# Kernel tuning notes

Measured on AMD Instinct MI355X. Metric: run time of the kernel, lower is better.

## Reference

```python
import jax, jax.numpy as jnp
import numpy as np

N_NODES = 50000


def gcn_conv(x, W, b, src, dst, ew, n):
    """PyG-style GCNConv: D^-1/2 (A+I) D^-1/2 X W + b with self-loops of weight 1."""
    h = x @ W                                   # [N, out]
    loop = jnp.arange(n, dtype=src.dtype)
    s = jnp.concatenate([src, loop])            # [E+N]
    d = jnp.concatenate([dst, loop])
    w = jnp.concatenate([ew, jnp.ones((n,), dtype=x.dtype)])
    deg = jax.ops.segment_sum(w, d, num_segments=n)
    dinv = jnp.where(deg > 0, jax.lax.rsqrt(deg), 0.0)
    norm = dinv[s] * w * dinv[d]                # [E+N]
    out = jax.ops.segment_sum(h[s] * norm[:, None], d, num_segments=n)
    return out + b


def setup_inputs() -> dict:
    key = jax.random.key(0)
    ks = jax.random.split(key, 12)
    in_feats, hidden = 128, 128
    half = hidden // 2
    E = 800000
    x = jax.random.normal(ks[0], (N_NODES, in_feats), dtype=jnp.float32)
    edge_index = jax.random.randint(ks[1], (2, E), 0, N_NODES, dtype=jnp.int64)
    edge_weight = jax.random.uniform(ks[2], (E,), dtype=jnp.float32)
    def lin(k, fan_in, shape):
        bound = 1.0 / np.sqrt(fan_in)
        return jax.random.uniform(k, shape, minval=-bound, maxval=bound, dtype=jnp.float32)
    return {
        "x": x,
        "edge_index": edge_index,
        "edge_weight": edge_weight,
        "W1": lin(ks[3], in_feats, (in_feats, hidden)),
        "b1": jnp.zeros((hidden,), jnp.float32),
        "W2": lin(ks[4], hidden, (hidden, hidden)),
        "b2": jnp.zeros((hidden,), jnp.float32),
        "Ws": lin(ks[5], in_feats, (in_feats, hidden)),
        "bs": lin(ks[6], in_feats, (hidden,)),
        "Wl": lin(ks[7], in_feats, (in_feats, half)),
        "bl": jnp.zeros((half,), jnp.float32),
        "Wl2": lin(ks[8], half, (half, 1)),
        "bl2": lin(ks[9], half, (1,)),
    }


def reference(x, edge_index, edge_weight, W1, b1, W2, b2, Ws, bs, Wl, bl, Wl2, bl2):
    n = x.shape[0]
    src, dst = edge_index[0], edge_index[1]
    # conv1 + ReLU over neighbors
    h_neighbors = jax.nn.relu(gcn_conv(x, W1, b1, src, dst, edge_weight, n))
    # leader score: GCNConv -> ReLU -> Linear(.,1) -> sigmoid, per node
    ls_h = jax.nn.relu(gcn_conv(x, Wl, bl, src, dst, edge_weight, n))
    leader_score = jax.nn.sigmoid(ls_h @ Wl2 + bl2)        # [N, 1]
    # gated fusion of self projection vs neighbor aggregation
    h_self_proj = x @ Ws + bs
    h_new = (1.0 - leader_score) * h_neighbors + leader_score * h_self_proj
    h_final = jax.nn.relu(gcn_conv(h_new, W2, b2, src, dst, edge_weight, n))
    return (h_final, leader_score)
```

## Files before the change

kernel.cpp:

```cpp
#include <hip/hip_runtime.h>
#include <math.h>

#define THREADS 256
#define ELLS 96
#define GEMM_YSTRIDE 104
#define NPHA 256
#define BSHIFT 7
#define NBMAX 392
#define BCAP 4096
#define PERMAX 3136
#define PMAX 5872
#define LMAX 736

typedef unsigned int uint32;
typedef unsigned long long ull64;
typedef __attribute__((ext_vector_type(8))) short bf16x8;
typedef __attribute__((ext_vector_type(4))) float f32x4;
typedef __attribute__((ext_vector_type(2))) float f32x2;

__device__ __forceinline__ unsigned short f2bf_rne(float x) {
  uint32 u = __float_as_uint(x);
  u += 0x7fffu + ((u >> 16) & 1u);
  return (unsigned short)(u >> 16);
}

__device__ __forceinline__ f32x2 dw2f2(uint32 d) {
  f32x2 r;
  r.x = __uint_as_float(d << 16);
  r.y = __uint_as_float(d & 0xffff0000u);
  return r;
}


__global__ __launch_bounds__(256) void prep_fused(uint32* __restrict__ gcnt, int n,
                                                  const float* __restrict__ W1, const float* __restrict__ Wl,
                                                  const float* __restrict__ Ws, const float* __restrict__ W2,
                                                  unsigned short* __restrict__ whi, unsigned short* __restrict__ wlo,
                                                  const float* __restrict__ x, unsigned short* __restrict__ xraw,
                                                  int nW) {
  int b = blockIdx.x;
  int t = threadIdx.x;
  if (b == 0) {
    for (int k = t; k < NBMAX; k += 256) gcnt[k] = 0u;
// ... 9 lines not shown
    else if (slot < 192) { W = Wl; ncol = slot - 128; ncols = 64;  }
    else if (slot < 320) { W = Ws; ncol = slot - 192; ncols = 128; }
    else                 { W = W2; ncol = slot - 320; ncols = 128; }
    float v = W[(size_t)k * ncols + ncol];
    unsigned short hi = f2bf_rne(v);
    float hif = __uint_as_float((uint32)hi << 16);
    unsigned short lo = f2bf_rne(v - hif);
    whi[idx] = hi;
    wlo[idx] = lo;
  } else {
    int i = (b - 1 - nW) * 256 + t;
    if (i >= n * 16) return;
    const float* px = x + (size_t)i * 8;
    float4 a = *(const float4*)px;
    float4 c = *(const float4*)(px + 4);
    ushort4 r0, r1;
    r0.x = f2bf_rne(a.x); r0.y = f2bf_rne(a.y); r0.z = f2bf_rne(a.z); r0.w = f2bf_rne(a.w);
    r1.x = f2bf_rne(c.x); r1.y = f2bf_rne(c.y); r1.z = f2bf_rne(c.z); r1.w = f2bf_rne(c.w);
    *(ushort4*)(xraw + (size_t)i * 8) = r0;
    *(ushort4*)(xraw + (size_t)i * 8 + 4) = r1;
  }
}


struct Chunk {
  const unsigned short* A;
  const unsigned short* whi;
  const unsigned short* wlo;
  const float* bias;
  void* out;
  int ostride;
  int obf16;
};
struct GemmArgs { Chunk c[5]; };

__device__ __forceinline__ void gemm_body(const Chunk& d, int M, int nTiles, int tile0, int tstride) {
  const unsigned short* A = d.A;
  int w = threadIdx.x >> 6, lane = threadIdx.x & 63;
  int n16 = lane & 15, quad = lane >> 4;

  bf16x8 Bh[4][4], Bl[4][4];
  {
    const unsigned short* wh = d.whi + (size_t)n16 * 128 + quad * 8;
    const unsigned short* wl = d.wlo + (size_t)n16 * 128 + quad * 8;
#pragma unroll
    for (int ct = 0; ct < 4; ct++)
#pragma unroll
      for (int ks = 0; ks < 4; ks++) {
        Bh[ct][ks] = *(const bf16x8*)(wh + ct * 16 * 128 + ks * 32);
        Bl[ct][ks] = *(const bf16x8*)(wl + ct * 16 * 128 + ks * 32);
      }
  }
  float bv[4];
#pragma unroll
  for (int ct = 0; ct < 4; ct++) bv[ct] = d.bias ? d.bias[ct * 16 + n16] : 0.f;

  int tile = tile0;
  bf16x8 av0[4], av1[4];
  if (tile < nTiles) {
    int bm = tile * 128;
    int r0 = bm + w * 32 + n16, r1 = r0 + 16;
    int r0c = r0 < M ? r0 : M - 1;
    int r1c = r1 < M ? r1 : M - 1;
    const unsigned short* a0 = A + (size_t)r0c * 128 + quad * 8;
    const unsigned short* a1 = A + (size_t)r1c * 128 + quad * 8;
#pragma unroll
    for (int ks = 0; ks < 4; ks++) {
// ... 30 lines not shown
#pragma unroll
      for (int ct = 0; ct < 4; ct++) {
        acc[0][ct] = __builtin_amdgcn_mfma_f32_16x16x32_bf16(av0[ks], Bh[ct][ks], acc[0][ct], 0, 0, 0);
        acc[0][ct] = __builtin_amdgcn_mfma_f32_16x16x32_bf16(av0[ks], Bl[ct][ks], acc[0][ct], 0, 0, 0);
        acc[1][ct] = __builtin_amdgcn_mfma_f32_16x16x32_bf16(av1[ks], Bh[ct][ks], acc[1][ct], 0, 0, 0);
        acc[1][ct] = __builtin_amdgcn_mfma_f32_16x16x32_bf16(av1[ks], Bl[ct][ks], acc[1][ct], 0, 0, 0);
      }

    int bm = tile * 128;
#pragma unroll
    for (int ct = 0; ct < 4; ct++) {
      int col = ct * 16 + n16;
#pragma unroll
      for (int rt = 0; rt < 2; rt++) {
#pragma unroll
        for (int reg = 0; reg < 4; reg++) {
          int row = bm + w * 32 + rt * 16 + quad * 4 + reg;
          if (row < M) {
            float v = acc[rt][ct][reg] + bv[ct];
            if (d.obf16)
              ((unsigned short*)d.out)[(size_t)row * d.ostride + col] = f2bf_rne(v);
            else
              ((float*)d.out)[(size_t)row * d.ostride + col] = v;
          }
        }
      }
    }

#pragma unroll
    for (int ks = 0; ks < 4; ks++) { av0[ks] = nv0[ks]; av1[ks] = nv1[ks]; }
  }
}

__global__ __launch_bounds__(256, 2) void gemm_v3(GemmArgs args, int M, int nTiles) {
  gemm_body(args.c[blockIdx.x], M, nTiles, blockIdx.y, gridDim.y);
}


__global__ __launch_bounds__(256, 2) void fused_sg(GemmArgs args, int M, int nTiles, int nGemm,
                                                   const int* __restrict__ ei, const float* __restrict__ ew,
                                                   uint32* __restrict__ gcnt, uint2* __restrict__ staging, int E) {
  __shared__ uint32 cntS[NBMAX], offS[NBMAX], gbS[NBMAX], curS[NBMAX];
  __shared__ unsigned short lineBk[LMAX];
  __shared__ uint2 sortedS[PMAX];
  __shared__ uint32 Ptot;

  int b = blockIdx.x;
  int gemmIdx = -1, phIdx = -1;
  int twice = NPHA * 2;
  if (b < twice) {
    if (b & 1) gemmIdx = b >> 1; else phIdx = b >> 1;
  } else {
    gemmIdx = NPHA + (b - twice);
  }

  if (phIdx >= 0) {
    int t = threadIdx.x;
    int per = (E + NPHA - 1) / NPHA;
    int start = phIdx * per;
    int end = start + per; if (end > E) end = E;
    for (int k = t; k < NBMAX; k += 256) cntS[k] = 0u;
    __syncthreads();
    for (int i = start + t; i < end; i += 256)
      atomicAdd(&cntS[(uint32)ei[E + i] >> BSHIFT], 1u);
    __syncthreads();
    if (t < 64) {
      uint32 carry = 0;
      for (int base = 0; base < NBMAX; base += 64) {
        int k = base + t;
        uint32 v = (k < NBMAX) ? ((cntS[k] + 7u) & ~7u) : 0u;
        uint32 s = v;
#pragma unroll
        for (int dd = 1; dd < 64; dd <<= 1) {
          uint32 o = __shfl_up(s, dd);
          if (t >= dd) s += o;
        }
        if (k < NBMAX) offS[k] = carry + s - v;
        carry += __shfl(s, 63);
      }
      if (t == 0) Ptot = carry;
    }
    __syncthreads();
    uint32 P = Ptot;
    for (int k = t; k < NBMAX; k += 256) {
      uint32 pc = (cntS[k] + 7u) & ~7u;
      gbS[k] = pc ? atomicAdd(&gcnt[k], pc) : 0u;
      curS[k] = 0u;
      uint32 l1 = (offS[k] + pc) >> 3;
      for (uint32 l = offS[k] >> 3; l < l1; l++) lineBk[l] = (unsigned short)k;
    }
    for (uint32 j = t; j < P; j += 256) sortedS[j] = make_uint2(0xFFFFFFFFu, 0u);
    __syncthreads();
    for (int i = start + t; i < end; i += 256) {
      int d = ei[E + i];
      int s = ei[i];
      float w = ew[i];
      int bk = d >> BSHIFT;
      uint32 pos = offS[bk] + atomicAdd(&curS[bk], 1u);
      sortedS[pos] = make_uint2(((uint32)(d & 127) << 24) | (uint32)s, __float_as_uint(w));
    }
    __syncthreads();
    for (uint32 j = t; j < P; j += 256) {
      int k = lineBk[j >> 3];
      uint32 idx = gbS[k] + (j - offS[k]);
      if (idx < BCAP)
        staging[(size_t)k * BCAP + idx] = sortedS[j];
    }
    return;
  }

  int chunkId = gemmIdx % 5;
  int ytile = gemmIdx / 5;
  gemm_body(args.c[chunkId], M, nTiles, ytile, GEMM_YSTRIDE);
}


__global__ __launch_bounds__(256) void phaseB_kernel(const uint2* __restrict__ staging,
                                                     const uint32* __restrict__ gcnt,
                                                     int2* __restrict__ ell,
                                                     float* __restrict__ dinv, int* __restrict__ cnt32, int n) {
  __shared__ uint32 cntL[128], sumL[128];
  int b = blockIdx.x;
  int t = threadIdx.x;
  if (t < 128) { cntL[t] = 0u; sumL[t] = 0u; }
  __syncthreads();
  uint32 cnt = gcnt[b]; if (cnt > BCAP) cnt = BCAP;
  const uint2* sb = staging + (size_t)b * BCAP;
  int dbase = b << BSHIFT;
  for (uint32 i = t; i < cnt; i += 256) {
    uint2 en = sb[i];
    if ((en.x >> 24) == 0xFFu) continue;
    int dl = (int)(en.x >> 24);
    int s = (int)(en.x & 0xffffffu);
    float w = __uint_as_float(en.y);
    uint32 fx = (uint32)(w * 8388608.0f + 0.5f);
    atomicAdd(&sumL[dl], fx);
    uint32 slot = atomicAdd(&cntL[dl], 1u);
    if (slot < ELLS)
      ell[(size_t)(dbase + dl) * ELLS + slot] = make_int2(s, __float_as_int(w));
  }
  __syncthreads();
  if (t < 128) {
    int d = dbase + t;
    if (d < n) {
      const float S = 1.1920928955078125e-7f;
      dinv[d] = rsqrtf(1.0f + (float)sumL[t] * S);
      uint32 c = cntL[t];
      cnt32[d] = (int)(c < ELLS ? c : ELLS);
    }
  }
}


__global__ __launch_bounds__(256) void conv1_fused(const unsigned short* __restrict__ h1,
                                                   const unsigned short* __restrict__ hl,
                                                   const int* __restrict__ cnt,
                                                   const int2* __restrict__ csr,
                                                   const float* __restrict__ dinv,
                                                   const float* __restrict__ b1, const float* __restrict__ bl,
                                                   const float* __restrict__ Wl2, const float* __restrict__ bl2,
                                                   const unsigned short* __restrict__ hself,
                                                   unsigned short* __restrict__ hnew_out,
                                                   float* __restrict__ leader_out, int nnodes) {
  int wave = threadIdx.x >> 6;
  int lane = threadIdx.x & 63;
  int node = blockIdx.x * 4 + wave;
  if (node >= nnodes) return;
  int g = lane >> 4, q = lane & 15;
  bool ql = q < 8;
  int hq = q & 7;
  int rs = node * ELLS;
  int n = cnt[node];
  float di = dinv[node];
  f32x2 dv2 = {di, di};

  f32x2 acc1[4] = {};
  f32x2 accl[4] = {};
  if (g == 0) {
    uint4 v = *(const uint4*)(h1 + (size_t)node * 128 + 8 * q);
    acc1[0] = dv2 * dw2f2(v.x); acc1[1] = dv2 * dw2f2(v.y);
    acc1[2] = dv2 * dw2f2(v.z); acc1[3] = dv2 * dw2f2(v.w);
    if (ql) {
      uint4 vl = *(const uint4*)(hl + (size_t)node * 64 + 8 * q);
      accl[0] = dv2 * dw2f2(vl.x); accl[1] = dv2 * dw2f2(vl.y);
      accl[2] = dv2 * dw2f2(vl.z); accl[3] = dv2 * dw2f2(vl.w);
    }
  }

  int e = g;
  for (; e + 4 < n; e += 8) {
    int2 en0 = csr[rs + e];
    int2 en1 = csr[rs + e + 4];
    float wz0 = __int_as_float(en0.y) * dinv[en0.x];
    float wz1 = __int_as_float(en1.y) * dinv[en1.x];
    f32x2 w0 = {wz0, wz0};
    f32x2 w1 = {wz1, wz1};
    uint4 a0 = *(const uint4*)(h1 + (size_t)en0.x * 128 + 8 * q);
    uint4 a1 = *(const uint4*)(h1 + (size_t)en1.x * 128 + 8 * q);
    int srcl = ql ? en0.x : en1.x;
    float wzl = ql ? wz0 : wz1;
    uint4 c0 = *(const uint4*)(hl + (size_t)srcl * 64 + 8 * hq);
    f32x2 wl2 = {wzl, wzl};
    accl[0] += wl2 * dw2f2(c0.x);
    accl[1] += wl2 * dw2f2(c0.y);
    accl[2] += wl2 * dw2f2(c0.z);
    accl[3] += wl2 * dw2f2(c0.w);
    acc1[0] += w0 * dw2f2(a0.x) + w1 * dw2f2(a1.x);
    acc1[1] += w0 * dw2f2(a0.y) + w1 * dw2f2(a1.y);
    acc1[2] += w0 * dw2f2(a0.z) + w1 * dw2f2(a1.z);
    acc1[3] += w0 * dw2f2(a0.w) + w1 * dw2f2(a1.w);
  }
  if (e < n) {
    int2 en = csr[rs + e];
    float wz0 = __int_as_float(en.y) * dinv[en.x];
    f32x2 w0 = {wz0, wz0};
    uint4 a0 = *(const uint4*)(h1 + (size_t)en.x * 128 + 8 * q);
    float wzl = ql ? wz0 : 0.f;
    uint4 c0 = *(const uint4*)(hl + (size_t)en.x * 64 + 8 * hq);
    f32x2 wl2 = {wzl, wzl};
    accl[0] += wl2 * dw2f2(c0.x);
    accl[1] += wl2 * dw2f2(c0.y);
    accl[2] += wl2 * dw2f2(c0.z);
    accl[3] += wl2 * dw2f2(c0.w);
    acc1[0] += w0 * dw2f2(a0.x);
    acc1[1] += w0 * dw2f2(a0.y);
    acc1[2] += w0 * dw2f2(a0.z);
    acc1[3] += w0 * dw2f2(a0.w);
  }

#pragma unroll
  for (int k = 0; k < 4; k++) {
    acc1[k].x += __shfl_xor(acc1[k].x, 16);
    acc1[k].y += __shfl_xor(acc1[k].y, 16);
    acc1[k].x += __shfl_xor(acc1[k].x, 32);
    acc1[k].y += __shfl_xor(acc1[k].y, 32);
    accl[k].x += __shfl_xor(accl[k].x, 16);
    accl[k].y += __shfl_xor(accl[k].y, 16);
    accl[k].x += __shfl_xor(accl[k].x, 32);
    accl[k].y += __shfl_xor(accl[k].y, 32);
    accl[k].x += __shfl_xor(accl[k].x, 8);
    accl[k].y += __shfl_xor(accl[k].y, 8);
  }

  float part = 0.f;
  if (ql) {
    float b[8], w2[8];
    *(float4*)&b[0] = *(const float4*)(bl + 8 * q);
    *(float4*)&b[4] = *(const float4*)(bl + 8 * q + 4);
    *(float4*)&w2[0] = *(const float4*)(Wl2 + 8 * q);
    *(float4*)&w2[4] = *(const float4*)(Wl2 + 8 * q + 4);
#pragma unroll
    for (int k = 0; k < 4; k++) {
      part += fmaxf(di * accl[k].x + b[2 * k], 0.f) * w2[2 * k];
      part += fmaxf(di * accl[k].y + b[2 * k + 1], 0.f) * w2[2 * k + 1];
    }
  }
  part += __shfl_xor(part, 1);
  part += __shfl_xor(part, 2);
  part += __shfl_xor(part, 4);
  float z = __shfl(part, 0) + bl2[0];
  float l = 1.f / (1.f + expf(-z));
  if (lane == 0) leader_out[node] = l;

  if (g == 0) {
    float b[8], r[8], hs[8];
    *(float4*)&b[0] = *(const float4*)(b1 + 8 * q);
    *(float4*)&b[4] = *(const float4*)(b1 + 8 * q + 4);
    uint4 hsv = *(const uint4*)(hself + (size_t)node * 128 + 8 * q);
    f32x2 h0 = dw2f2(hsv.x), h1v = dw2f2(hsv.y), h2v = dw2f2(hsv.z), h3v = dw2f2(hsv.w);
    hs[0] = h0.x; hs[1] = h0.y; hs[2] = h1v.x; hs[3] = h1v.y;
    hs[4] = h2v.x; hs[5] = h2v.y; hs[6] = h3v.x; hs[7] = h3v.y;
    float a[8];
    a[0] = acc1[0].x; a[1] = acc1[0].y; a[2] = acc1[1].x; a[3] = acc1[1].y;
    a[4] = acc1[2].x; a[5] = acc1[2].y; a[6] = acc1[3].x; a[7] = acc1[3].y;
#pragma unroll
    for (int j = 0; j < 8; j++) {
      r[j] = fmaxf(di * a[j] + b[j], 0.f);
      r[j] = (1.f - l) * r[j] + l * hs[j];
      r[j] *= di;
    }
    ushort4 p0, p1;
    p0.x = f2bf_rne(r[0]); p0.y = f2bf_rne(r[1]); p0.z = f2bf_rne(r[2]); p0.w = f2bf_rne(r[3]);
    p1.x = f2bf_rne(r[4]); p1.y = f2bf_rne(r[5]); p1.z = f2bf_rne(r[6]); p1.w = f2bf_rne(r[7]);
    *(ushort4*)(hnew_out + (size_t)node * 128 + 8 * q) = p0;
    *(ushort4*)(hnew_out + (size_t)node * 128 + 8 * q + 4) = p1;
  }
}


__global__ __launch_bounds__(256) void agg_conv2_kernel(const unsigned short* __restrict__ h,
                                                        const int* __restrict__ cnt,
                                                        const int2* __restrict__ csr,
                                                        const float* __restrict__ dinv, const float* __restrict__ bias,
                                                        float* __restrict__ out, int nnodes) {
  int wave = threadIdx.x >> 6;
  int lane = threadIdx.x & 63;
  int node = blockIdx.x * 4 + wave;
  if (node >= nnodes) return;
  int g = lane >> 4;
  int q = lane & 15;
  int rs = node * ELLS;
  int n = cnt[node];
  float di = dinv[node];

  f32x2 acc[4] = {};
  if (g == 0) {
    uint4 v = *(const uint4*)(h + (size_t)node * 128 + 8 * q);
    acc[0] = dw2f2(v.x); acc[1] = dw2f2(v.y);
    acc[2] = dw2f2(v.z); acc[3] = dw2f2(v.w);
  }
  int e = g;
  for (; e + 4 < n; e += 8) {
    int2 en0 = csr[rs + e];
    int2 en1 = csr[rs + e + 4];
    f32x2 w0 = {__int_as_float(en0.y), __int_as_float(en0.y)};
    f32x2 w1 = {__int_as_float(en1.y), __int_as_float(en1.y)};
    uint4 v0 = *(const uint4*)(h + (size_t)en0.x * 128 + 8 * q);
    uint4 v1 = *(const uint4*)(h + (size_t)en1.x * 128 + 8 * q);
// ... 36 lines not shown
extern "C" void kernel_launch(void* const* d_in, const int* in_sizes, int n_in,
                              void* d_out, int out_size, void* d_ws, size_t ws_size,
                              hipStream_t stream) {
  const float* x   = (const float*)d_in[0];
  const int*   ei  = (const int*)d_in[1];
  const float* ew  = (const float*)d_in[2];
  const float* W1  = (const float*)d_in[3];
  const float* b1  = (const float*)d_in[4];
  const float* W2  = (const float*)d_in[5];
  const float* b2  = (const float*)d_in[6];
  const float* Wsp = (const float*)d_in[7];
  const float* bs  = (const float*)d_in[8];
  const float* Wl  = (const float*)d_in[9];
  const float* bl  = (const float*)d_in[10];
  const float* Wl2 = (const float*)d_in[11];
  const float* bl2 = (const float*)d_in[12];

  const int N = in_sizes[0] / 128;
  const int E = in_sizes[1] / 2;
  const int NB = (N + 127) >> BSHIFT;

  char* ws = (char*)d_ws;
  size_t off = 0;
  auto alloc = [&](size_t bytes) -> void* {
    void* p = ws + off;
    off = (off + bytes + 255) & ~(size_t)255;
    return p;
  };
  uint32* gcnt     = (uint32*)alloc((size_t)NBMAX * 4);
  uint2* staging   = (uint2*)alloc((size_t)NBMAX * BCAP * 8);
  float* dinv      = (float*)alloc((size_t)N * 4);
  int*   cnt32     = (int*)alloc((size_t)N * 4);
  int2*  ell       = (int2*)alloc((size_t)N * ELLS * 8);
  unsigned short* xraw   = (unsigned short*)alloc((size_t)N * 128 * 2);
  unsigned short* h1bf   = (unsigned short*)alloc((size_t)N * 128 * 2);
  unsigned short* hlbf   = (unsigned short*)alloc((size_t)N * 64 * 2);
  unsigned short* hnewbf = (unsigned short*)alloc((size_t)N * 128 * 2);
  unsigned short* hspbf  = (unsigned short*)alloc((size_t)N * 128 * 2);
  unsigned short* whi = (unsigned short*)alloc((size_t)448 * 128 * 2);
  unsigned short* wlo = (unsigned short*)alloc((size_t)448 * 128 * 2);

  float* h_final = (float*)d_out;
  float* leader  = (float*)d_out + (size_t)N * 128;

  int gWave = (N + 3) / 4;
  int nTiles = (N + 127) / 128;
  int nCast = (N * 16 + 255) / 256;
  int nW = (448 * 128 + 255) / 256;

  prep_fused<<<1 + nW + nCast, 256, 0, stream>>>(gcnt, N, W1, Wl, Wsp, W2, whi, wlo, x, xraw, nW);

  {
    GemmArgs ga;
    ga.c[0] = {xraw, whi + 0 * 128,   wlo + 0 * 128,   nullptr, h1bf,       128, 1};
    ga.c[1] = {xraw, whi + 64 * 128,  wlo + 64 * 128,  nullptr, h1bf + 64,  128, 1};
    ga.c[2] = {xraw, whi + 128 * 128, wlo + 128 * 128, nullptr, hlbf,       64,  1};
    ga.c[3] = {xraw, whi + 192 * 128, wlo + 192 * 128, bs,      hspbf,      128, 1};
    ga.c[4] = {xraw, whi + 256 * 128, wlo + 256 * 128, bs + 64, hspbf + 64, 128, 1};
    int nGemm = 5 * GEMM_YSTRIDE;
    int totalBlocks = NPHA * 2 + (nGemm - NPHA);
    fused_sg<<<totalBlocks, 256, 0, stream>>>(ga, N, nTiles, nGemm, ei, ew, gcnt, staging, E);
  }

  phaseB_kernel<<<NB, 256, 0, stream>>>(staging, gcnt, ell, dinv, cnt32, N);

  conv1_fused<<<gWave, 256, 0, stream>>>(h1bf, hlbf, cnt32, ell, dinv,
                                         b1, bl, Wl2, bl2, hspbf, hnewbf, leader, N);

  {
    GemmArgs ga;
    ga.c[0] = {hnewbf, whi + 320 * 128, wlo + 320 * 128, nullptr, h1bf,      128, 1};
    ga.c[1] = {hnewbf, whi + 384 * 128, wlo + 384 * 128, nullptr, h1bf + 64, 128, 1};
    ga.c[2] = ga.c[0]; ga.c[3] = ga.c[0]; ga.c[4] = ga.c[0];
    gemm_v3<<<dim3(2, 256), 256, 0, stream>>>(ga, N, nTiles);
  }
  agg_conv2_kernel<<<gWave, 256, 0, stream>>>(h1bf, cnt32, ell,
                                              dinv, b2, h_final, N);
}
```

Measured before the change: 254.0 us.

## Fuse conv2 GEMM into conv1 aggregation epilogue via LDS tile and MFMA

The conv1 aggregation kernel now processes 16 nodes per block and stages the gated h_new rows in shared memory. It then multiplies them by W2 with bf16 MFMA (hi/lo split) directly, writing h2. This drops the separate GEMM launch and the round trip of h_new through global memory. In exchange, each block reloads the W2 fragments from global memory and adds a block barrier, and each wave now serially handles four nodes, so less latency is hidden per wave.

```diff
diff --git a/kernel.cpp b/kernel.cpp
--- a/kernel.cpp
+++ b/kernel.cpp
@@ -8,7 +8,6 @@
 #define BSHIFT 7
 #define NBMAX 392
 #define BCAP 4096
-#define PERMAX 3136
 #define PMAX 5872
 #define LMAX 736
 
@@ -181,10 +180,6 @@
   }
 }
 
-__global__ __launch_bounds__(256, 2) void gemm_v3(GemmArgs args, int M, int nTiles) {
-  gemm_body(args.c[blockIdx.x], M, nTiles, blockIdx.y, gridDim.y);
-}
-
 
 __global__ __launch_bounds__(256, 2) void fused_sg(GemmArgs args, int M, int nTiles, int nGemm,
                                                    const int* __restrict__ ei, const float* __restrict__ ew,
@@ -301,138 +296,180 @@
 }
 
 
-__global__ __launch_bounds__(256) void conv1_fused(const unsigned short* __restrict__ h1,
-                                                   const unsigned short* __restrict__ hl,
-                                                   const int* __restrict__ cnt,
-                                                   const int2* __restrict__ csr,
-                                                   const float* __restrict__ dinv,
-                                                   const float* __restrict__ b1, const float* __restrict__ bl,
-                                                   const float* __restrict__ Wl2, const float* __restrict__ bl2,
-                                                   const unsigned short* __restrict__ hself,
-                                                   unsigned short* __restrict__ hnew_out,
-                                                   float* __restrict__ leader_out, int nnodes) {
+__global__ __launch_bounds__(256) void conv1_g2(const unsigned short* __restrict__ h1,
+                                                const unsigned short* __restrict__ hl,
+                                                const int* __restrict__ cnt,
+                                                const int2* __restrict__ csr,
+                                                const float* __restrict__ dinv,
+                                                const float* __restrict__ b1, const float* __restrict__ bl,
+                                                const float* __restrict__ Wl2, const float* __restrict__ bl2,
+                                                const unsigned short* __restrict__ hself,
+                                                const unsigned short* __restrict__ whi,
+                                                const unsigned short* __restrict__ wlo,
+                                                unsigned short* __restrict__ h2_out,
+                                                float* __restrict__ leader_out, int nnodes) {
+  __shared__ unsigned short hn[16][136];
+  int blk = blockIdx.x;
   int wave = threadIdx.x >> 6;
   int lane = threadIdx.x & 63;
-  int node = blockIdx.x * 4 + wave;
-  if (node >= nnodes) return;
   int g = lane >> 4, q = lane & 15;
   bool ql = q < 8;
   int hq = q & 7;
-  int rs = node * ELLS;
-  int n = cnt[node];
-  float di = dinv[node];
-  f32x2 dv2 = {di, di};
-
-  f32x2 acc1[4] = {};
-  f32x2 accl[4] = {};
-  if (g == 0) {
-    uint4 v = *(const uint4*)(h1 + (size_t)node * 128 + 8 * q);
-    acc1[0] = dv2 * dw2f2(v.x); acc1[1] = dv2 * dw2f2(v.y);
-    acc1[2] = dv2 * dw2f2(v.z); acc1[3] = dv2 * dw2f2(v.w);
+
+  for (int i = 0; i < 4; i++) {
+    int node = blk * 16 + wave * 4 + i;
+    if (node >= nnodes) break;
+    int rs = node * ELLS;
+    int n = cnt[node];
+    float di = dinv[node];
+    f32x2 dv2 = {di, di};
+
+    f32x2 acc1[4] = {};
+    f32x2 accl[4] = {};
+    if (g == 0) {
+      uint4 v = *(const uint4*)(h1 + (size_t)node * 128 + 8 * q);
+      acc1[0] = dv2 * dw2f2(v.x); acc1[1] = dv2 * dw2f2(v.y);
+      acc1[2] = dv2 * dw2f2(v.z); acc1[3] = dv2 * dw2f2(v.w);
+      if (ql) {
+        uint4 vl = *(const uint4*)(hl + (size_t)node * 64 + 8 * q);
+        accl[0] = dv2 * dw2f2(vl.x); accl[1] = dv2 * dw2f2(vl.y);
+        accl[2] = dv2 * dw2f2(vl.z); accl[3] = dv2 * dw2f2(vl.w);
+      }
+    }
+
+    int e = g;
+    for (; e + 4 < n; e += 8) {
+      int2 en0 = csr[rs + e];
+      int2 en1 = csr[rs + e + 4];
+      float wz0 = __int_as_float(en0.y) * dinv[en0.x];
+      float wz1 = __int_as_float(en1.y) * dinv[en1.x];
+      f32x2 w0 = {wz0, wz0};
+      f32x2 w1 = {wz1, wz1};
+      uint4 a0 = *(const uint4*)(h1 + (size_t)en0.x * 128 + 8 * q);
+      uint4 a1 = *(const uint4*)(h1 + (size_t)en1.x * 128 + 8 * q);
+      int srcl = ql ? en0.x : en1.x;
+      float wzl = ql ? wz0 : wz1;
+      uint4 c0 = *(const uint4*)(hl + (size_t)srcl * 64 + 8 * hq);
+      f32x2 wl2v = {wzl, wzl};
+      accl[0] += wl2v * dw2f2(c0.x);
+      accl[1] += wl2v * dw2f2(c0.y);
+      accl[2] += wl2v * dw2f2(c0.z);
+      accl[3] += wl2v * dw2f2(c0.w);
+      acc1[0] += w0 * dw2f2(a0.x) + w1 * dw2f2(a1.x);
+      acc1[1] += w0 * dw2f2(a0.y) + w1 * dw2f2(a1.y);
+      acc1[2] += w0 * dw2f2(a0.z) + w1 * dw2f2(a1.z);
+      acc1[3] += w0 * dw2f2(a0.w) + w1 * dw2f2(a1.w);
+    }
+    if (e < n) {
+      int2 en = csr[rs + e];
+      float wz0 = __int_as_float(en.y) * dinv[en.x];
+      f32x2 w0 = {wz0, wz0};
+      uint4 a0 = *(const uint4*)(h1 + (size_t)en.x * 128 + 8 * q);
+      float wzl = ql ? wz0 : 0.f;
+      uint4 c0 = *(const uint4*)(hl + (size_t)en.x * 64 + 8 * hq);
+      f32x2 wl2v = {wzl, wzl};
+      accl[0] += wl2v * dw2f2(c0.x);
+      accl[1] += wl2v * dw2f2(c0.y);
+      accl[2] += wl2v * dw2f2(c0.z);
+      accl[3] += wl2v * dw2f2(c0.w);
+      acc1[0] += w0 * dw2f2(a0.x);
+      acc1[1] += w0 * dw2f2(a0.y);
+      acc1[2] += w0 * dw2f2(a0.z);
+      acc1[3] += w0 * dw2f2(a0.w);
+    }
+
+#pragma unroll
+    for (int k = 0; k < 4; k++) {
+      acc1[k].x += __shfl_xor(acc1[k].x, 16);
+      acc1[k].y += __shfl_xor(acc1[k].y, 16);
+      acc1[k].x += __shfl_xor(acc1[k].x, 32);
+      acc1[k].y += __shfl_xor(acc1[k].y, 32);
+      accl[k].x += __shfl_xor(accl[k].x, 16);
+      accl[k].y += __shfl_xor(accl[k].y, 16);
+      accl[k].x += __shfl_xor(accl[k].x, 32);
+      accl[k].y += __shfl_xor(accl[k].y, 32);
+      accl[k].x += __shfl_xor(accl[k].x, 8);
+      accl[k].y += __shfl_xor(accl[k].y, 8);
+    }
+
+    float part = 0.f;
     if (ql) {
-      uint4 vl = *(const uint4*)(hl + (size_t)node * 64 + 8 * q);
-      accl[0] = dv2 * dw2f2(vl.x); accl[1] = dv2 * dw2f2(vl.y);
-      accl[2] = dv2 * dw2f2(vl.z); accl[3] = dv2 * dw2f2(vl.w);
-    }
-  }
-
-  int e = g;
-  for (; e + 4 < n; e += 8) {
-    int2 en0 = csr[rs + e];
-    int2 en1 = csr[rs + e + 4];
-    float wz0 = __int_as_float(en0.y) * dinv[en0.x];
-    float wz1 = __int_as_float(en1.y) * dinv[en1.x];
-    f32x2 w0 = {wz0, wz0};
-    f32x2 w1 = {wz1, wz1};
-    uint4 a0 = *(const uint4*)(h1 + (size_t)en0.x * 128 + 8 * q);
-    uint4 a1 = *(const uint4*)(h1 + (size_t)en1.x * 128 + 8 * q);
-    int srcl = ql ? en0.x : en1.x;
-    float wzl = ql ? wz0 : wz1;
-    uint4 c0 = *(const uint4*)(hl + (size_t)srcl * 64 + 8 * hq);
-    f32x2 wl2 = {wzl, wzl};
-    accl[0] += wl2 * dw2f2(c0.x);
-    accl[1] += wl2 * dw2f2(c0.y);
-    accl[2] += wl2 * dw2f2(c0.z);
-    accl[3] += wl2 * dw2f2(c0.w);
-    acc1[0] += w0 * dw2f2(a0.x) + w1 * dw2f2(a1.x);
-    acc1[1] += w0 * dw2f2(a0.y) + w1 * dw2f2(a1.y);
-    acc1[2] += w0 * dw2f2(a0.z) + w1 * dw2f2(a1.z);
-    acc1[3] += w0 * dw2f2(a0.w) + w1 * dw2f2(a1.w);
-  }
-  if (e < n) {
-    int2 en = csr[rs + e];
-    float wz0 = __int_as_float(en.y) * dinv[en.x];
-    f32x2 w0 = {wz0, wz0};
-    uint4 a0 = *(const uint4*)(h1 + (size_t)en.x * 128 + 8 * q);
-    float wzl = ql ? wz0 : 0.f;
-    uint4 c0 = *(const uint4*)(hl + (size_t)en.x * 64 + 8 * hq);
-    f32x2 wl2 = {wzl, wzl};
-    accl[0] += wl2 * dw2f2(c0.x);
-    accl[1] += wl2 * dw2f2(c0.y);
-    accl[2] += wl2 * dw2f2(c0.z);
-    accl[3] += wl2 * dw2f2(c0.w);
-    acc1[0] += w0 * dw2f2(a0.x);
-    acc1[1] += w0 * dw2f2(a0.y);
-    acc1[2] += w0 * dw2f2(a0.z);
-    acc1[3] += w0 * dw2f2(a0.w);
-  }
-
-#pragma unroll
-  for (int k = 0; k < 4; k++) {
-    acc1[k].x += __shfl_xor(acc1[k].x, 16);
-    acc1[k].y += __shfl_xor(acc1[k].y, 16);
-    acc1[k].x += __shfl_xor(acc1[k].x, 32);
-    acc1[k].y += __shfl_xor(acc1[k].y, 32);
-    accl[k].x += __shfl_xor(accl[k].x, 16);
-    accl[k].y += __shfl_xor(accl[k].y, 16);
-    accl[k].x += __shfl_xor(accl[k].x, 32);
-    accl[k].y += __shfl_xor(accl[k].y, 32);
-    accl[k].x += __shfl_xor(accl[k].x, 8);
-    accl[k].y += __shfl_xor(accl[k].y, 8);
-  }
-
-  float part = 0.f;
-  if (ql) {
-    float b[8], w2[8];
-    *(float4*)&b[0] = *(const float4*)(bl + 8 * q);
-    *(float4*)&b[4] = *(const float4*)(bl + 8 * q + 4);
-    *(float4*)&w2[0] = *(const float4*)(Wl2 + 8 * q);
-    *(float4*)&w2[4] = *(const float4*)(Wl2 + 8 * q + 4);
-#pragma unroll
-    for (int k = 0; k < 4; k++) {
-      part += fmaxf(di * accl[k].x + b[2 * k], 0.f) * w2[2 * k];
-      part += fmaxf(di * accl[k].y + b[2 * k + 1], 0.f) * w2[2 * k + 1];
-    }
-  }
-  part += __shfl_xor(part, 1);
-  part += __shfl_xor(part, 2);
-  part += __shfl_xor(part, 4);
-  float z = __shfl(part, 0) + bl2[0];
-  float l = 1.f / (1.f + expf(-z));
-  if (lane == 0) leader_out[node] = l;
-
-  if (g == 0) {
-    float b[8], r[8], hs[8];
-    *(float4*)&b[0] = *(const float4*)(b1 + 8 * q);
-    *(float4*)&b[4] = *(const float4*)(b1 + 8 * q + 4);
-    uint4 hsv = *(const uint4*)(hself + (size_t)node * 128 + 8 * q);
-    f32x2 h0 = dw2f2(hsv.x), h1v = dw2f2(hsv.y), h2v = dw2f2(hsv.z), h3v = dw2f2(hsv.w);
-    hs[0] = h0.x; hs[1] = h0.y; hs[2] = h1v.x; hs[3] = h1v.y;
-    hs[4] = h2v.x; hs[5] = h2v.y; hs[6] = h3v.x; hs[7] = h3v.y;
-    float a[8];
-    a[0] = acc1[0].x; a[1] = acc1[0].y; a[2] = acc1[1].x; a[3] = acc1[1].y;
-    a[4] = acc1[2].x; a[5] = acc1[2].y; a[6] = acc1[3].x; a[7] = acc1[3].y;
-#pragma unroll
-    for (int j = 0; j < 8; j++) {
-      r[j] = fmaxf(di * a[j] + b[j], 0.f);
-      r[j] = (1.f - l) * r[j] + l * hs[j];
-      r[j] *= di;
-    }
-    ushort4 p0, p1;
-    p0.x = f2bf_rne(r[0]); p0.y = f2bf_rne(r[1]); p0.z = f2bf_rne(r[2]); p0.w = f2bf_rne(r[3]);
-    p1.x = f2bf_rne(r[4]); p1.y = f2bf_rne(r[5]); p1.z = f2bf_rne(r[6]); p1.w = f2bf_rne(r[7]);
-    *(ushort4*)(hnew_out + (size_t)node * 128 + 8 * q) = p0;
-    *(ushort4*)(hnew_out + (size_t)node * 128 + 8 * q + 4) = p1;
+      float b[8], w2[8];
+      *(float4*)&b[0] = *(const float4*)(bl + 8 * q);
+      *(float4*)&b[4] = *(const float4*)(bl + 8 * q + 4);
+      *(float4*)&w2[0] = *(const float4*)(Wl2 + 8 * q);
+      *(float4*)&w2[4] = *(const float4*)(Wl2 + 8 * q + 4);
+#pragma unroll
+      for (int k = 0; k < 4; k++) {
+        part += fmaxf(di * accl[k].x + b[2 * k], 0.f) * w2[2 * k];
+        part += fmaxf(di * accl[k].y + b[2 * k + 1], 0.f) * w2[2 * k + 1];
+      }
+    }
+    part += __shfl_xor(part, 1);
+    part += __shfl_xor(part, 2);
+    part += __shfl_xor(part, 4);
+    float z = __shfl(part, 0) + bl2[0];
+    float l = 1.f / (1.f + expf(-z));
+    if (lane == 0) leader_out[node] = l;
+
+    if (g == 0) {
+      float b[8], rr[8], hs[8];
+      *(float4*)&b[0] = *(const float4*)(b1 + 8 * q);
+      *(float4*)&b[4] = *(const float4*)(b1 + 8 * q + 4);
+      uint4 hsv = *(const uint4*)(hself + (size_t)node * 128 + 8 * q);
+      f32x2 h0 = dw2f2(hsv.x), h1v = dw2f2(hsv.y), h2v = dw2f2(hsv.z), h3v = dw2f2(hsv.w);
+      hs[0] = h0.x; hs[1] = h0.y; hs[2] = h1v.x; hs[3] = h1v.y;
+      hs[4] = h2v.x; hs[5] = h2v.y; hs[6] = h3v.x; hs[7] = h3v.y;
+      float a[8];
+      a[0] = acc1[0].x; a[1] = acc1[0].y; a[2] = acc1[1].x; a[3] = acc1[1].y;
+      a[4] = acc1[2].x; a[5] = acc1[2].y; a[6] = acc1[3].x; a[7] = acc1[3].y;
+#pragma unroll
+      for (int j = 0; j < 8; j++) {
+        rr[j] = fmaxf(di * a[j] + b[j], 0.f);
+        rr[j] = (1.f - l) * rr[j] + l * hs[j];
+        rr[j] *= di;
+      }
+      uint4 pv;
+      pv.x = (uint32)f2bf_rne(rr[0]) | ((uint32)f2bf_rne(rr[1]) << 16);
+      pv.y = (uint32)f2bf_rne(rr[2]) | ((uint32)f2bf_rne(rr[3]) << 16);
+      pv.z = (uint32)f2bf_rne(rr[4]) | ((uint32)f2bf_rne(rr[5]) << 16);
+      pv.w = (uint32)f2bf_rne(rr[6]) | ((uint32)f2bf_rne(rr[7]) << 16);
+      *(uint4*)&hn[wave * 4 + i][8 * q] = pv;
+    }
+  }
+  __syncthreads();
+
+  {
+    int n16 = lane & 15, quad = lane >> 4;
+    bf16x8 av[4];
+#pragma unroll
+    for (int ks = 0; ks < 4; ks++)
+      av[ks] = *(const bf16x8*)&hn[n16][quad * 8 + ks * 32];
+#pragma unroll
+    for (int tci = 0; tci < 2; tci++) {
+      int ct = wave * 2 + tci;
+      const unsigned short* wh = whi + (size_t)(320 + ct * 16 + n16) * 128 + quad * 8;
+      const unsigned short* wl = wlo + (size_t)(320 + ct * 16 + n16) * 128 + quad * 8;
+      bf16x8 Bh[4], Bl[4];
+#pragma unroll
+      for (int ks = 0; ks < 4; ks++) {
+        Bh[ks] = *(const bf16x8*)(wh + ks * 32);
+        Bl[ks] = *(const bf16x8*)(wl + ks * 32);
+      }
+      f32x4 acc = {0.f, 0.f, 0.f, 0.f};
+#pragma unroll
+      for (int ks = 0; ks < 4; ks++) {
+        acc = __builtin_amdgcn_mfma_f32_16x16x32_bf16(av[ks], Bh[ks], acc, 0, 0, 0);
+        acc = __builtin_amdgcn_mfma_f32_16x16x32_bf16(av[ks], Bl[ks], acc, 0, 0, 0);
+      }
+      int col = ct * 16 + n16;
+#pragma unroll
+      for (int reg = 0; reg < 4; reg++) {
+        int row = blk * 16 + quad * 4 + reg;
+        if (row < nnodes)
+          h2_out[(size_t)row * 128 + col] = f2bf_rne(acc[reg]);
+      }
+    }
   }
 }
 
@@ -538,7 +575,7 @@
   unsigned short* xraw   = (unsigned short*)alloc((size_t)N * 128 * 2);
   unsigned short* h1bf   = (unsigned short*)alloc((size_t)N * 128 * 2);
   unsigned short* hlbf   = (unsigned short*)alloc((size_t)N * 64 * 2);
-  unsigned short* hnewbf = (unsigned short*)alloc((size_t)N * 128 * 2);
+  unsigned short* h2bf   = (unsigned short*)alloc((size_t)N * 128 * 2);
   unsigned short* hspbf  = (unsigned short*)alloc((size_t)N * 128 * 2);
   unsigned short* whi = (unsigned short*)alloc((size_t)448 * 128 * 2);
   unsigned short* wlo = (unsigned short*)alloc((size_t)448 * 128 * 2);
@@ -550,6 +587,7 @@
   int nTiles = (N + 127) / 128;
   int nCast = (N * 16 + 255) / 256;
   int nW = (448 * 128 + 255) / 256;
+  int gConv = (N + 15) / 16;
 
   prep_fused<<<1 + nW + nCast, 256, 0, stream>>>(gcnt, N, W1, Wl, Wsp, W2, whi, wlo, x, xraw, nW);
 
@@ -567,16 +605,9 @@
 
   phaseB_kernel<<<NB, 256, 0, stream>>>(staging, gcnt, ell, dinv, cnt32, N);
 
-  conv1_fused<<<gWave, 256, 0, stream>>>(h1bf, hlbf, cnt32, ell, dinv,
-                                         b1, bl, Wl2, bl2, hspbf, hnewbf, leader, N);
-
-  {
-    GemmArgs ga;
-    ga.c[0] = {hnewbf, whi + 320 * 128, wlo + 320 * 128, nullptr, h1bf,      128, 1};
-    ga.c[1] = {hnewbf, whi + 384 * 128, wlo + 384 * 128, nullptr, h1bf + 64, 128, 1};
-    ga.c[2] = ga.c[0]; ga.c[3] = ga.c[0]; ga.c[4] = ga.c[0];
-    gemm_v3<<<dim3(2, 256), 256, 0, stream>>>(ga, N, nTiles);
-  }
-  agg_conv2_kernel<<<gWave, 256, 0, stream>>>(h1bf, cnt32, ell,
+  conv1_g2<<<gConv, 256, 0, stream>>>(h1bf, hlbf, cnt32, ell, dinv,
+                                      b1, bl, Wl2, bl2, hspbf, whi, wlo, h2bf, leader, N);
+
+  agg_conv2_kernel<<<gWave, 256, 0, stream>>>(h2bf, cnt32, ell,
                                               dinv, b2, h_final, N);
 }
```

After: 266.9 us. 5.1% more time.

## Aggregate raw features before GEMM and fuse conv1, leader gate, and conv2 GEMM

Applied to the files above, without the earlier changes.

Uses linearity to reorder conv1 as (A_hat X) W instead of A_hat (X W). A single gather over X now feeds both the W1 and Wl projections, instead of gathering h1 and hl separately. A new fused GEMM kernel computes the leader score, the gated mix with the self projection, and the W2 projection per 128-row tile, with h_new kept in shared memory. This removes one full-size intermediate round trip and a kernel launch, and shrinks the first fused scatter/GEMM launch to only the self projection. The trade-off is lower GEMM parallelism (one block per tile doing three GEMMs serially) and bf16 rounding of the aggregated input rather than of h.

```diff
diff --git a/kernel.cpp b/kernel.cpp
--- a/kernel.cpp
+++ b/kernel.cpp
@@ -8,7 +8,6 @@
 #define BSHIFT 7
 #define NBMAX 392
 #define BCAP 4096
-#define PERMAX 3136
 #define PMAX 5872
 #define LMAX 736
 
@@ -84,7 +83,7 @@
   int ostride;
   int obf16;
 };
-struct GemmArgs { Chunk c[5]; };
+struct GemmArgs { Chunk c[2]; };
 
 __device__ __forceinline__ void gemm_body(const Chunk& d, int M, int nTiles, int tile0, int tstride) {
   const unsigned short* A = d.A;
@@ -181,10 +180,6 @@
   }
 }
 
-__global__ __launch_bounds__(256, 2) void gemm_v3(GemmArgs args, int M, int nTiles) {
-  gemm_body(args.c[blockIdx.x], M, nTiles, blockIdx.y, gridDim.y);
-}
-
 
 __global__ __launch_bounds__(256, 2) void fused_sg(GemmArgs args, int M, int nTiles, int nGemm,
                                                    const int* __restrict__ ei, const float* __restrict__ ew,
@@ -196,11 +191,11 @@
 
   int b = blockIdx.x;
   int gemmIdx = -1, phIdx = -1;
-  int twice = NPHA * 2;
+  int twice = nGemm * 2;
   if (b < twice) {
     if (b & 1) gemmIdx = b >> 1; else phIdx = b >> 1;
   } else {
-    gemmIdx = NPHA + (b - twice);
+    phIdx = nGemm + (b - twice);
   }
 
   if (phIdx >= 0) {
@@ -258,8 +253,8 @@
     return;
   }
 
-  int chunkId = gemmIdx % 5;
-  int ytile = gemmIdx / 5;
+  int chunkId = gemmIdx & 1;
+  int ytile = gemmIdx >> 1;
   gemm_body(args.c[chunkId], M, nTiles, ytile, GEMM_YSTRIDE);
 }
 
@@ -301,41 +296,27 @@
 }
 
 
-__global__ __launch_bounds__(256) void conv1_fused(const unsigned short* __restrict__ h1,
-                                                   const unsigned short* __restrict__ hl,
+__global__ __launch_bounds__(256) void aggx_kernel(const unsigned short* __restrict__ xr,
                                                    const int* __restrict__ cnt,
                                                    const int2* __restrict__ csr,
                                                    const float* __restrict__ dinv,
-                                                   const float* __restrict__ b1, const float* __restrict__ bl,
-                                                   const float* __restrict__ Wl2, const float* __restrict__ bl2,
-                                                   const unsigned short* __restrict__ hself,
-                                                   unsigned short* __restrict__ hnew_out,
-                                                   float* __restrict__ leader_out, int nnodes) {
+                                                   unsigned short* __restrict__ z, int nnodes) {
   int wave = threadIdx.x >> 6;
   int lane = threadIdx.x & 63;
   int node = blockIdx.x * 4 + wave;
   if (node >= nnodes) return;
   int g = lane >> 4, q = lane & 15;
-  bool ql = q < 8;
-  int hq = q & 7;
   int rs = node * ELLS;
   int n = cnt[node];
   float di = dinv[node];
   f32x2 dv2 = {di, di};
 
-  f32x2 acc1[4] = {};
-  f32x2 accl[4] = {};
+  f32x2 acc[4] = {};
   if (g == 0) {
-    uint4 v = *(const uint4*)(h1 + (size_t)node * 128 + 8 * q);
-    acc1[0] = dv2 * dw2f2(v.x); acc1[1] = dv2 * dw2f2(v.y);
-    acc1[2] = dv2 * dw2f2(v.z); acc1[3] = dv2 * dw2f2(v.w);
-    if (ql) {
-      uint4 vl = *(const uint4*)(hl + (size_t)node * 64 + 8 * q);
-      accl[0] = dv2 * dw2f2(vl.x); accl[1] = dv2 * dw2f2(vl.y);
-      accl[2] = dv2 * dw2f2(vl.z); accl[3] = dv2 * dw2f2(vl.w);
-    }
-  }
-
+    uint4 v = *(const uint4*)(xr + (size_t)node * 128 + 8 * q);
+    acc[0] = dv2 * dw2f2(v.x); acc[1] = dv2 * dw2f2(v.y);
+    acc[2] = dv2 * dw2f2(v.z); acc[3] = dv2 * dw2f2(v.w);
+  }
   int e = g;
   for (; e + 4 < n; e += 8) {
     int2 en0 = csr[rs + e];
@@ -344,95 +325,182 @@
     float wz1 = __int_as_float(en1.y) * dinv[en1.x];
     f32x2 w0 = {wz0, wz0};
     f32x2 w1 = {wz1, wz1};
-    uint4 a0 = *(const uint4*)(h1 + (size_t)en0.x * 128 + 8 * q);
-    uint4 a1 = *(const uint4*)(h1 + (size_t)en1.x * 128 + 8 * q);
-    int srcl = ql ? en0.x : en1.x;
-    float wzl = ql ? wz0 : wz1;
-    uint4 c0 = *(const uint4*)(hl + (size_t)srcl * 64 + 8 * hq);
-    f32x2 wl2 = {wzl, wzl};
-    accl[0] += wl2 * dw2f2(c0.x);
-    accl[1] += wl2 * dw2f2(c0.y);
-    accl[2] += wl2 * dw2f2(c0.z);
-    accl[3] += wl2 * dw2f2(c0.w);
-    acc1[0] += w0 * dw2f2(a0.x) + w1 * dw2f2(a1.x);
-    acc1[1] += w0 * dw2f2(a0.y) + w1 * dw2f2(a1.y);
-    acc1[2] += w0 * dw2f2(a0.z) + w1 * dw2f2(a1.z);
-    acc1[3] += w0 * dw2f2(a0.w) + w1 * dw2f2(a1.w);
+    uint4 a0 = *(const uint4*)(xr + (size_t)en0.x * 128 + 8 * q);
+    uint4 a1 = *(const uint4*)(xr + (size_t)en1.x * 128 + 8 * q);
+    acc[0] += w0 * dw2f2(a0.x) + w1 * dw2f2(a1.x);
+    acc[1] += w0 * dw2f2(a0.y) + w1 * dw2f2(a1.y);
+    acc[2] += w0 * dw2f2(a0.z) + w1 * dw2f2(a1.z);
+    acc[3] += w0 * dw2f2(a0.w) + w1 * dw2f2(a1.w);
   }
   if (e < n) {
     int2 en = csr[rs + e];
     float wz0 = __int_as_float(en.y) * dinv[en.x];
     f32x2 w0 = {wz0, wz0};
-    uint4 a0 = *(const uint4*)(h1 + (size_t)en.x * 128 + 8 * q);
-    float wzl = ql ? wz0 : 0.f;
-    uint4 c0 = *(const uint4*)(hl + (size_t)en.x * 64 + 8 * hq);
-    f32x2 wl2 = {wzl, wzl};
-    accl[0] += wl2 * dw2f2(c0.x);
-    accl[1] += wl2 * dw2f2(c0.y);
-    accl[2] += wl2 * dw2f2(c0.z);
-    accl[3] += wl2 * dw2f2(c0.w);
-    acc1[0] += w0 * dw2f2(a0.x);
-    acc1[1] += w0 * dw2f2(a0.y);
-    acc1[2] += w0 * dw2f2(a0.z);
-    acc1[3] += w0 * dw2f2(a0.w);
-  }
-
+    uint4 a0 = *(const uint4*)(xr + (size_t)en.x * 128 + 8 * q);
+    acc[0] += w0 * dw2f2(a0.x);
+    acc[1] += w0 * dw2f2(a0.y);
+    acc[2] += w0 * dw2f2(a0.z);
+    acc[3] += w0 * dw2f2(a0.w);
+  }
 #pragma unroll
   for (int k = 0; k < 4; k++) {
-    acc1[k].x += __shfl_xor(acc1[k].x, 16);
-    acc1[k].y += __shfl_xor(acc1[k].y, 16);
-    acc1[k].x += __shfl_xor(acc1[k].x, 32);
-    acc1[k].y += __shfl_xor(acc1[k].y, 32);
-    accl[k].x += __shfl_xor(accl[k].x, 16);
-    accl[k].y += __shfl_xor(accl[k].y, 16);
-    accl[k].x += __shfl_xor(accl[k].x, 32);
-    accl[k].y += __shfl_xor(accl[k].y, 32);
-    accl[k].x += __shfl_xor(accl[k].x, 8);
-    accl[k].y += __shfl_xor(accl[k].y, 8);
-  }
-
-  float part = 0.f;
-  if (ql) {
-    float b[8], w2[8];
-    *(float4*)&b[0] = *(const float4*)(bl + 8 * q);
-    *(float4*)&b[4] = *(const float4*)(bl + 8 * q + 4);
-    *(float4*)&w2[0] = *(const float4*)(Wl2 + 8 * q);
-    *(float4*)&w2[4] = *(const float4*)(Wl2 + 8 * q + 4);
-#pragma unroll
-    for (int k = 0; k < 4; k++) {
-      part += fmaxf(di * accl[k].x + b[2 * k], 0.f) * w2[2 * k];
-      part += fmaxf(di * accl[k].y + b[2 * k + 1], 0.f) * w2[2 * k + 1];
-    }
-  }
-  part += __shfl_xor(part, 1);
-  part += __shfl_xor(part, 2);
-  part += __shfl_xor(part, 4);
-  float z = __shfl(part, 0) + bl2[0];
-  float l = 1.f / (1.f + expf(-z));
-  if (lane == 0) leader_out[node] = l;
-
+    acc[k].x += __shfl_xor(acc[k].x, 16);
+    acc[k].y += __shfl_xor(acc[k].y, 16);
+    acc[k].x += __shfl_xor(acc[k].x, 32);
+    acc[k].y += __shfl_xor(acc[k].y, 32);
+  }
   if (g == 0) {
-    float b[8], r[8], hs[8];
-    *(float4*)&b[0] = *(const float4*)(b1 + 8 * q);
-    *(float4*)&b[4] = *(const float4*)(b1 + 8 * q + 4);
-    uint4 hsv = *(const uint4*)(hself + (size_t)node * 128 + 8 * q);
-    f32x2 h0 = dw2f2(hsv.x), h1v = dw2f2(hsv.y), h2v = dw2f2(hsv.z), h3v = dw2f2(hsv.w);
-    hs[0] = h0.x; hs[1] = h0.y; hs[2] = h1v.x; hs[3] = h1v.y;
-    hs[4] = h2v.x; hs[5] = h2v.y; hs[6] = h3v.x; hs[7] = h3v.y;
-    float a[8];
-    a[0] = acc1[0].x; a[1] = acc1[0].y; a[2] = acc1[1].x; a[3] = acc1[1].y;
-    a[4] = acc1[2].x; a[5] = acc1[2].y; a[6] = acc1[3].x; a[7] = acc1[3].y;
-#pragma unroll
-    for (int j = 0; j < 8; j++) {
-      r[j] = fmaxf(di * a[j] + b[j], 0.f);
-      r[j] = (1.f - l) * r[j] + l * hs[j];
-      r[j] *= di;
-    }
+    float r[8];
+    r[0] = di * acc[0].x; r[1] = di * acc[0].y; r[2] = di * acc[1].x; r[3] = di * acc[1].y;
+    r[4] = di * acc[2].x; r[5] = di * acc[2].y; r[6] = di * acc[3].x; r[7] = di * acc[3].y;
     ushort4 p0, p1;
     p0.x = f2bf_rne(r[0]); p0.y = f2bf_rne(r[1]); p0.z = f2bf_rne(r[2]); p0.w = f2bf_rne(r[3]);
     p1.x = f2bf_rne(r[4]); p1.y = f2bf_rne(r[5]); p1.z = f2bf_rne(r[6]); p1.w = f2bf_rne(r[7]);
-    *(ushort4*)(hnew_out + (size_t)node * 128 + 8 * q) = p0;
-    *(ushort4*)(hnew_out + (size_t)node * 128 + 8 * q + 4) = p1;
+    *(ushort4*)(z + (size_t)node * 128 + 8 * q) = p0;
+    *(ushort4*)(z + (size_t)node * 128 + 8 * q + 4) = p1;
+  }
+}
+
+
+__global__ __launch_bounds__(256) void gemm_fused(const unsigned short* __restrict__ z,
+                                                  const unsigned short* __restrict__ hsp,
+                                                  const unsigned short* __restrict__ whi,
+                                                  const unsigned short* __restrict__ wlo,
+                                                  const float* __restrict__ b1, const float* __restrict__ bl,
+                                                  const float* __restrict__ Wl2, const float* __restrict__ bl2,
+                                                  const float* __restrict__ dinv,
+                                                  unsigned short* __restrict__ h2_out,
+                                                  float* __restrict__ leader_out, int n) {
+  __shared__ unsigned short hn[128][136];
+  int tile = blockIdx.x;
+  int w = threadIdx.x >> 6, lane = threadIdx.x & 63;
+  int n16 = lane & 15, quad = lane >> 4;
+  int bm = tile * 128;
+
+  bf16x8 av[2][4];
+#pragma unroll
+  for (int rt = 0; rt < 2; rt++) {
+    int r = bm + w * 32 + rt * 16 + n16;
+    int rc = r < n ? r : n - 1;
+    const unsigned short* a = z + (size_t)rc * 128 + quad * 8;
+#pragma unroll
+    for (int ks = 0; ks < 4; ks++) av[rt][ks] = *(const bf16x8*)(a + ks * 32);
+  }
+
+  float lgate[2][4];
+  {
+    f32x4 ls[2][4];
+#pragma unroll
+    for (int rt = 0; rt < 2; rt++)
+#pragma unroll
+      for (int cf = 0; cf < 4; cf++) ls[rt][cf] = (f32x4){0.f, 0.f, 0.f, 0.f};
+#pragma unroll
+    for (int cf = 0; cf < 4; cf++) {
+      const unsigned short* wh = whi + (size_t)(128 + cf * 16 + n16) * 128 + quad * 8;
+      const unsigned short* wl = wlo + (size_t)(128 + cf * 16 + n16) * 128 + quad * 8;
+#pragma unroll
+      for (int ks = 0; ks < 4; ks++) {
+        bf16x8 Bh = *(const bf16x8*)(wh + ks * 32);
+        bf16x8 Bl = *(const bf16x8*)(wl + ks * 32);
+        ls[0][cf] = __builtin_amdgcn_mfma_f32_16x16x32_bf16(av[0][ks], Bh, ls[0][cf], 0, 0, 0);
+        ls[0][cf] = __builtin_amdgcn_mfma_f32_16x16x32_bf16(av[0][ks], Bl, ls[0][cf], 0, 0, 0);
+        ls[1][cf] = __builtin_amdgcn_mfma_f32_16x16x32_bf16(av[1][ks], Bh, ls[1][cf], 0, 0, 0);
+        ls[1][cf] = __builtin_amdgcn_mfma_f32_16x16x32_bf16(av[1][ks], Bl, ls[1][cf], 0, 0, 0);
+      }
+    }
+#pragma unroll
+    for (int rt = 0; rt < 2; rt++)
+#pragma unroll
+      for (int reg = 0; reg < 4; reg++) {
+        float p = 0.f;
+#pragma unroll
+        for (int cf = 0; cf < 4; cf++) {
+          int col = cf * 16 + n16;
+          p += fmaxf(ls[rt][cf][reg] + bl[col], 0.f) * Wl2[col];
+        }
+        p += __shfl_xor(p, 1);
+        p += __shfl_xor(p, 2);
+        p += __shfl_xor(p, 4);
+        p += __shfl_xor(p, 8);
+        float lv = 1.f / (1.f + expf(-(p + bl2[0])));
+        lgate[rt][reg] = lv;
+        int row = bm + w * 32 + rt * 16 + quad * 4 + reg;
+        if (n16 == 0 && row < n) leader_out[row] = lv;
+      }
+  }
+
+  float dirr[2][4];
+#pragma unroll
+  for (int rt = 0; rt < 2; rt++)
+#pragma unroll
+    for (int reg = 0; reg < 4; reg++) {
+      int row = bm + w * 32 + rt * 16 + quad * 4 + reg;
+      dirr[rt][reg] = row < n ? dinv[row] : 0.f;
+    }
+
+#pragma unroll
+  for (int cf = 0; cf < 8; cf++) {
+    f32x4 h0 = {0.f, 0.f, 0.f, 0.f}, h1v = {0.f, 0.f, 0.f, 0.f};
+    const unsigned short* wh = whi + (size_t)(cf * 16 + n16) * 128 + quad * 8;
+    const unsigned short* wl = wlo + (size_t)(cf * 16 + n16) * 128 + quad * 8;
+#pragma unroll
+    for (int ks = 0; ks < 4; ks++) {
+      bf16x8 Bh = *(const bf16x8*)(wh + ks * 32);
+      bf16x8 Bl = *(const bf16x8*)(wl + ks * 32);
+      h0 = __builtin_amdgcn_mfma_f32_16x16x32_bf16(av[0][ks], Bh, h0, 0, 0, 0);
+      h0 = __builtin_amdgcn_mfma_f32_16x16x32_bf16(av[0][ks], Bl, h0, 0, 0, 0);
+      h1v = __builtin_amdgcn_mfma_f32_16x16x32_bf16(av[1][ks], Bh, h1v, 0, 0, 0);
+      h1v = __builtin_amdgcn_mfma_f32_16x16x32_bf16(av[1][ks], Bl, h1v, 0, 0, 0);
+    }
+    int col = cf * 16 + n16;
+    float bc = b1[col];
+#pragma unroll
+    for (int rt = 0; rt < 2; rt++) {
+      f32x4 a = rt ? h1v : h0;
+#pragma unroll
+      for (int reg = 0; reg < 4; reg++) {
+        int row = bm + w * 32 + rt * 16 + quad * 4 + reg;
+        int rc = row < n ? row : n - 1;
+        float hs = __uint_as_float((uint32)hsp[(size_t)rc * 128 + col] << 16);
+        float rl = fmaxf(a[reg] + bc, 0.f);
+        float lv = lgate[rt][reg];
+        float hv = ((1.f - lv) * rl + lv * hs) * dirr[rt][reg];
+        hn[w * 32 + rt * 16 + quad * 4 + reg][col] = f2bf_rne(hv);
+      }
+    }
+  }
+  __syncthreads();
+
+  bf16x8 av2[2][4];
+#pragma unroll
+  for (int rt = 0; rt < 2; rt++)
+#pragma unroll
+    for (int ks = 0; ks < 4; ks++)
+      av2[rt][ks] = *(const bf16x8*)&hn[w * 32 + rt * 16 + n16][quad * 8 + ks * 32];
+#pragma unroll
+  for (int cf = 0; cf < 8; cf++) {
+    f32x4 h0 = {0.f, 0.f, 0.f, 0.f}, h1v = {0.f, 0.f, 0.f, 0.f};
+    const unsigned short* wh = whi + (size_t)(320 + cf * 16 + n16) * 128 + quad * 8;
+    const unsigned short* wl = wlo + (size_t)(320 + cf * 16 + n16) * 128 + quad * 8;
+#pragma unroll
+    for (int ks = 0; ks < 4; ks++) {
+      bf16x8 Bh = *(const bf16x8*)(wh + ks * 32);
+      bf16x8 Bl = *(const bf16x8*)(wl + ks * 32);
+      h0 = __builtin_amdgcn_mfma_f32_16x16x32_bf16(av2[0][ks], Bh, h0, 0, 0, 0);
+      h0 = __builtin_amdgcn_mfma_f32_16x16x32_bf16(av2[0][ks], Bl, h0, 0, 0, 0);
+      h1v = __builtin_amdgcn_mfma_f32_16x16x32_bf16(av2[1][ks], Bh, h1v, 0, 0, 0);
+      h1v = __builtin_amdgcn_mfma_f32_16x16x32_bf16(av2[1][ks], Bl, h1v, 0, 0, 0);
+    }
+    int col = cf * 16 + n16;
+#pragma unroll
+    for (int rt = 0; rt < 2; rt++) {
+      f32x4 a = rt ? h1v : h0;
+#pragma unroll
+      for (int reg = 0; reg < 4; reg++) {
+        int row = bm + w * 32 + rt * 16 + quad * 4 + reg;
+        if (row < n) h2_out[(size_t)row * 128 + col] = f2bf_rne(a[reg]);
+      }
+    }
   }
 }
 
@@ -535,11 +603,10 @@
   float* dinv      = (float*)alloc((size_t)N * 4);
   int*   cnt32     = (int*)alloc((size_t)N * 4);
   int2*  ell       = (int2*)alloc((size_t)N * ELLS * 8);
-  unsigned short* xraw   = (unsigned short*)alloc((size_t)N * 128 * 2);
-  unsigned short* h1bf   = (unsigned short*)alloc((size_t)N * 128 * 2);
-  unsigned short* hlbf   = (unsigned short*)alloc((size_t)N * 64 * 2);
-  unsigned short* hnewbf = (unsigned short*)alloc((size_t)N * 128 * 2);
-  unsigned short* hspbf  = (unsigned short*)alloc((size_t)N * 128 * 2);
+  unsigned short* xraw  = (unsigned short*)alloc((size_t)N * 128 * 2);
+  unsigned short* zbf   = (unsigned short*)alloc((size_t)N * 128 * 2);
+  unsigned short* h2bf  = (unsigned short*)alloc((size_t)N * 128 * 2);
+  unsigned short* hspbf = (unsigned short*)alloc((size_t)N * 128 * 2);
   unsigned short* whi = (unsigned short*)alloc((size_t)448 * 128 * 2);
   unsigned short* wlo = (unsigned short*)alloc((size_t)448 * 128 * 2);
 
@@ -555,28 +622,20 @@
 
   {
     GemmArgs ga;
-    ga.c[0] = {xraw, whi + 0 * 128,   wlo + 0 * 128,   nullptr, h1bf,       128, 1};
-    ga.c[1] = {xraw, whi + 64 * 128,  wlo + 64 * 128,  nullptr, h1bf + 64,  128, 1};
-    ga.c[2] = {xraw, whi + 128 * 128, wlo + 128 * 128, nullptr, hlbf,       64,  1};
-    ga.c[3] = {xraw, whi + 192 * 128, wlo + 192 * 128, bs,      hspbf,      128, 1};
-    ga.c[4] = {xraw, whi + 256 * 128, wlo + 256 * 128, bs + 64, hspbf + 64, 128, 1};
-    int nGemm = 5 * GEMM_YSTRIDE;
-    int totalBlocks = NPHA * 2 + (nGemm - NPHA);
+    ga.c[0] = {xraw, whi + 192 * 128, wlo + 192 * 128, bs,      hspbf,      128, 1};
+    ga.c[1] = {xraw, whi + 256 * 128, wlo + 256 * 128, bs + 64, hspbf + 64, 128, 1};
+    int nGemm = 2 * GEMM_YSTRIDE;
+    int totalBlocks = NPHA + nGemm;
     fused_sg<<<totalBlocks, 256, 0, stream>>>(ga, N, nTiles, nGemm, ei, ew, gcnt, staging, E);
   }
 
   phaseB_kernel<<<NB, 256, 0, stream>>>(staging, gcnt, ell, dinv, cnt32, N);
 
-  conv1_fused<<<gWave, 256, 0, stream>>>(h1bf, hlbf, cnt32, ell, dinv,
-                                         b1, bl, Wl2, bl2, hspbf, hnewbf, leader, N);
-
-  {
-    GemmArgs ga;
-    ga.c[0] = {hnewbf, whi + 320 * 128, wlo + 320 * 128, nullptr, h1bf,      128, 1};
-    ga.c[1] = {hnewbf, whi + 384 * 128, wlo + 384 * 128, nullptr, h1bf + 64, 128, 1};
-    ga.c[2] = ga.c[0]; ga.c[3] = ga.c[0]; ga.c[4] = ga.c[0];
-    gemm_v3<<<dim3(2, 256), 256, 0, stream>>>(ga, N, nTiles);
-  }
-  agg_conv2_kernel<<<gWave, 256, 0, stream>>>(h1bf, cnt32, ell,
+  aggx_kernel<<<gWave, 256, 0, stream>>>(xraw, cnt32, ell, dinv, zbf, N);
+
+  gemm_fused<<<nTiles, 256, 0, stream>>>(zbf, hspbf, whi, wlo, b1, bl, Wl2, bl2,
+                                         dinv, h2bf, leader, N);
+
+  agg_conv2_kernel<<<gWave, 256, 0, stream>>>(h2bf, cnt32, ell,
                                               dinv, b2, h_final, N);
 }
```

New measurement: 252.3 us. Within noise of the previous version (-0.7%).
